# Optimization experiments

Hardware: AMD Instinct MI355X
Metric: run time of the kernel (lower is better)

Reference implementation:

```python
import jax, jax.numpy as jnp
import numpy as np

TEMPERATURE = 0.2
NUM_CLASSES = 80  # background label == NUM_CLASSES
M, K, B = 8192, 128, 60


def setup_inputs() -> dict:
    key = jax.random.key(0)
    k1, k2, k3 = jax.random.split(key, 3)
    feats = jax.random.normal(k1, (M, K), dtype=jnp.float32)
    feats = feats / jnp.linalg.norm(feats, axis=-1, keepdims=True)
    protos = jax.random.normal(k2, (B, K), dtype=jnp.float32)
    protos = protos / jnp.linalg.norm(protos, axis=-1, keepdims=True)
    labels = jax.random.randint(k3, (M,), 0, NUM_CLASSES + 1)  # NUM_CLASSES == bg
    proto_labels = jnp.arange(B, dtype=jnp.int64 if jax.config.read('jax_enable_x64') else jnp.int32)
    return {"features": feats, "labels": labels, "protos": protos, "proto_labels": proto_labels}


def reference(features, labels, protos, proto_labels):
    # masked (fixed-shape) formulation of the original boolean-gather code
    fg = labels != NUM_CLASSES                                   # [M]
    is_base = fg & jnp.any(labels[None, :] == proto_labels[:, None], axis=0)
    is_novel = fg & ~is_base
    nf = is_novel.astype(features.dtype)                         # [M] novel mask
    bf = is_base.astype(features.dtype)                          # [M] base mask
    numel = jnp.sum(fg).astype(features.dtype)

    sim = jnp.matmul(features, features.T) / TEMPERATURE          # [M,M]
    pk = jnp.matmul(features, protos.T) / TEMPERATURE             # [M,B]
    exp_sim = jnp.exp(sim)                                        # [M,M]
    eye = jnp.eye(features.shape[0], dtype=features.dtype)
    offdiag = (1.0 - eye)

    # ---- novel branch: rows i with is_novel[i] ----
    # denom: sum over novel j != i of exp(sim) + sum over protos of RAW pk (faithful to source)
    exp_nn_sum = jnp.sum(exp_sim * nf[None, :] * offdiag, axis=1)  # [M]
    denom_n = exp_nn_sum + jnp.sum(pk, axis=1)                     # [M]
    log_prob = sim - jnp.log(denom_n)[:, None]
    # novel_label_mask in source is elementwise labels==labels -> all True
    n_novel = jnp.sum(nf)
    cnt = jnp.maximum(n_novel - 1.0, 1.0)                          # per-row positive count
    per_row_novel = -jnp.sum(log_prob * nf[None, :] * offdiag, axis=1) / cnt
    loss_novel = jnp.sum(per_row_novel * nf)
    loss_novel = jnp.where(n_novel > 1.0, loss_novel, 0.0)

    # ---- base branch: rows i with is_base[i] ----
    safe_lab = jnp.clip(labels, 0, protos.shape[0] - 1)
    pi = jnp.einsum('nc,nc->n', features, protos[safe_lab]) / TEMPERATURE  # [M]
    denom_b = jnp.sum(exp_sim * nf[None, :], axis=1) + jnp.sum(jnp.exp(pk), axis=1)
    loss_base = jnp.sum(bf * -(pi - jnp.log(denom_b)))
    loss_base = jnp.where(jnp.any(is_base), loss_base, 0.0)

    return (loss_novel + loss_base) / numel
```

## Files before the change

kernel.cpp:

```cpp
#include <hip/hip_runtime.h>
#include <math.h>

#define NCLS 80
#define KDIM 128
#define INV_T 5.0f
#define AST 136
#define BST 72

typedef __attribute__((ext_vector_type(4))) float  floatx4;
typedef __attribute__((ext_vector_type(8))) short  short8;

__device__ inline unsigned short f2bf(float x) {
    unsigned int u = __float_as_uint(x);
    u += 0x7fffu + ((u >> 16) & 1u);
    return (unsigned short)(u >> 16);
}
__device__ inline ushort4 pack4(float4 v) {
    ushort4 r; r.x = f2bf(v.x); r.y = f2bf(v.y); r.z = f2bf(v.z); r.w = f2bf(v.w);
    return r;
}

__global__ __launch_bounds__(256) void setup_kernel(
    const int* __restrict__ labels, int M, int B,
    int* __restrict__ novel_idx, int* __restrict__ counters,
    float* __restrict__ S1, float* __restrict__ T1,
    float* __restrict__ PKr, float* __restrict__ EK, float* __restrict__ out)
{
    int i = blockIdx.x * 256 + threadIdx.x;
    if (i == 0) out[0] = 0.f;
    if (i >= M) return;
    S1[i] = 0.f; T1[i] = 0.f; PKr[i] = 0.f; EK[i] = 0.f;
    int lab = labels[i];
    bool fg  = (lab != NCLS);
    bool isb = fg && (lab >= 0) && (lab < B);
    bool isn = fg && !isb;
    if (isn) { int p = atomicAdd(&counters[0], 1); novel_idx[p] = i; }
    if (fg)  atomicAdd(&counters[1], 1);
    if (isb) atomicAdd(&counters[2], 1);
}

__global__ __launch_bounds__(256, 2) void gemm_kernel(
    const float* __restrict__ feats, const float* __restrict__ protos,
    const int* __restrict__ novel_idx, const int* __restrict__ counters,
    int M, int B,
    float* __restrict__ S1, float* __restrict__ T1,
    float* __restrict__ PKr, float* __restrict__ EK)
{
    __shared__ unsigned short As[128 * AST];
    __shared__ unsigned short Bs[128 * BST];
    __shared__ int nidx[128];

    const int Nn = counters[0];
    const int ntiles = (Nn + 127) >> 7;
    const int ct = blockIdx.x >> 6;
    const int rt = blockIdx.x & 63;
    if (ct > ntiles) return;
    const bool isproto = (ct == ntiles);
    const int row0 = rt * 128;
    const int tid = threadIdx.x;

    {
        const float4* f4 = (const float4*)(feats + (size_t)row0 * KDIM);
        #pragma unroll
        for (int p = 0; p < 16; ++p) {
            int chunk = p * 256 + tid;
            int r = chunk >> 5, kc = chunk & 31;
            float4 v = f4[r * 32 + kc];
            *(ushort4*)&As[r * AST + kc * 4] = pack4(v);
        }
    }

    const int wave = tid >> 6;
    const int lane = tid & 63;
    const int lr   = lane & 15;
    const int quad = lane >> 4;
    const int wrow = (wave >> 1) * 64;
    const int wcol = (wave & 1) * 64;

    floatx4 acc[4][4];
    #pragma unroll
    for (int r = 0; r < 4; ++r)
        #pragma unroll
        for (int c = 0; c < 4; ++c)
            acc[r][c] = (floatx4){0.f, 0.f, 0.f, 0.f};

    for (int h = 0; h < 2; ++h) {
        if (h) __syncthreads();
        #pragma unroll
        for (int p = 0; p < 8; ++p) {
            int chunk = p * 256 + tid;
            int r = chunk >> 4, kc = chunk & 15;
            float4 v = make_float4(0.f, 0.f, 0.f, 0.f);
            if (isproto) {
                if (r < B) v = *(const float4*)(protos + (size_t)r * KDIM + h * 64 + kc * 4);
            } else {
                int jg = ct * 128 + r;
                if (jg < Nn) {
                    int nid = novel_idx[jg];
                    v = *(const float4*)(feats + (size_t)nid * KDIM + h * 64 + kc * 4);
                }
            }
            *(ushort4*)&Bs[r * BST + kc * 4] = pack4(v);
        }
        if (h == 0 && tid < 128) {
            int nid = -1;
            if (isproto) { if (tid < B) nid = tid; }
            else { int jg = ct * 128 + tid; if (jg < Nn) nid = novel_idx[jg]; }
            nidx[tid] = nid;
        }
        __syncthreads();
        #pragma unroll
        for (int ks = 0; ks < 2; ++ks) {
            short8 a[4], b[4];
            #pragma unroll
            for (int r = 0; r < 4; ++r)
                a[r] = *(const short8*)&As[(wrow + r * 16 + lr) * AST + h * 64 + ks * 32 + quad * 8];
            #pragma unroll
            for (int c = 0; c < 4; ++c)
                b[c] = *(const short8*)&Bs[(wcol + c * 16 + lr) * BST + ks * 32 + quad * 8];
            #pragma unroll
            for (int r = 0; r < 4; ++r)
                #pragma unroll
                for (int c = 0; c < 4; ++c)
                    acc[r][c] = __builtin_amdgcn_mfma_f32_16x16x32_bf16(
                        a[r], b[c], acc[r][c], 0, 0, 0);
        }
    }

    int ncol[4];
    #pragma unroll
    for (int c = 0; c < 4; ++c) ncol[c] = nidx[wcol + c * 16 + lr];

    #pragma unroll
    for (int r = 0; r < 4; ++r) {
        int ibase = row0 + wrow + r * 16 + quad * 4;
        #pragma unroll
        for (int reg = 0; reg < 4; ++reg) {
            int irow = ibase + reg;
            float se = 0.f, sr = 0.f;
            #pragma unroll
            for (int c = 0; c < 4; ++c) {
                float sim = acc[r][c][reg] * INV_T;
                bool valid = (ncol[c] >= 0) && (isproto || ncol[c] != irow);
                if (valid) { se += __expf(sim); sr += sim; }
            }
            #pragma unroll
            for (int off = 1; off < 16; off <<= 1) {
                se += __shfl_xor(se, off);
                sr += __shfl_xor(sr, off);
            }
            if (lr == 0) {
                if (isproto) { atomicAdd(&EK[irow], se); atomicAdd(&PKr[irow], sr); }
                else         { atomicAdd(&S1[irow], se); atomicAdd(&T1[irow], sr); }
            }
        }
    }
}

__global__ __launch_bounds__(256) void finalize_kernel(
    const float* __restrict__ feats, const float* __restrict__ protos,
    const int* __restrict__ labels,
    const float* __restrict__ S1, const float* __restrict__ T1,
    const float* __restrict__ PKr, const float* __restrict__ EK,
    const int* __restrict__ counters, int M, int B, float* __restrict__ out)
{
    __shared__ float part[16];
    const int tid  = threadIdx.x;
    const int rloc = tid >> 4;
    const int q    = tid & 15;
    const int row  = blockIdx.x * 16 + rloc;
    const int rs   = min(row, M - 1);

    const int Nn = counters[0], numel = counters[1], nbase = counters[2];

    int lab = labels[rs];
    bool fg  = (lab != NCLS);
    bool isb = fg && (lab >= 0) && (lab < B);
    bool isn = fg && !isb;
    int  sl  = min(max(lab, 0), B - 1);

    float d = 0.f;
    #pragma unroll
    for (int j = 0; j < 8; ++j) {
        int k = q + j * 16;
        d += feats[(size_t)rs * KDIM + k] * protos[(size_t)sl * KDIM + k];
    }
    #pragma unroll
    for (int off = 1; off < 16; off <<= 1) d += __shfl_xor(d, off);

    if (q == 0) {
        float loss = 0.f;
        if (row < M) {
            if (isn && Nn > 1) {
                float cnt = (float)(Nn - 1);
                float dn  = S1[rs] + PKr[rs];
                loss = -(T1[rs] - cnt * logf(dn)) / cnt;
            } else if (isb && nbase > 0) {
                float pi = d * INV_T;
                float db = S1[rs] + EK[rs];
                loss = -(pi - logf(db));
            }
        }
        part[rloc] = loss;
    }
    __syncthreads();
    if (tid == 0) {
        float s = 0.f;
        #pragma unroll
        for (int r = 0; r < 16; ++r) s += part[r];
        atomicAdd(out, s / (float)numel);
    }
}

extern "C" void kernel_launch(void* const* d_in, const int* in_sizes, int n_in,
                              void* d_out, int out_size, void* d_ws, size_t ws_size,
                              hipStream_t stream)
{
    const float* feats  = (const float*)d_in[0];
    const int*   labels = (const int*)d_in[1];
    const float* protos = (const float*)d_in[2];

    const int M = in_sizes[1];
    const int B = in_sizes[3];

    char* ws = (char*)d_ws;
    int*   counters  = (int*)ws;
    float* S1  = (float*)(ws + 64);
    float* T1  = S1 + M;
    float* PKr = T1 + M;
    float* EK  = PKr + M;
    int*   novel_idx = (int*)(EK + M);

    hipMemsetAsync(counters, 0, 64, stream);

    setup_kernel<<<(M + 255) / 256, 256, 0, stream>>>(
        labels, M, B, novel_idx, counters, S1, T1, PKr, EK, (float*)d_out);

    int rowTiles = (M + 127) / 128;
    int maxct    = (M + 127) / 128;
    gemm_kernel<<<rowTiles * (maxct + 1), 256, 0, stream>>>(
        feats, protos, novel_idx, counters, M, B, S1, T1, PKr, EK);

    finalize_kernel<<<(M + 15) / 16, 256, 0, stream>>>(
        feats, protos, labels, S1, T1, PKr, EK, counters, M, B, (float*)d_out);
}
```

Baseline: 106.9 us.

## Fuse finalize into gemm via last-block reduction and single-block setup

```diff
diff --git a/kernel.cpp b/kernel.cpp
--- a/kernel.cpp
+++ b/kernel.cpp
@@ -5,7 +5,7 @@
 #define KDIM 128
 #define INV_T 5.0f
 #define AST 136
-#define BST 72
+#define BST 68
 
 typedef __attribute__((ext_vector_type(4))) float  floatx4;
 typedef __attribute__((ext_vector_type(8))) short  short8;
@@ -20,195 +20,232 @@
     return r;
 }
 
-__global__ __launch_bounds__(256) void setup_kernel(
+__global__ __launch_bounds__(1024) void setup_kernel(
     const int* __restrict__ labels, int M, int B,
     int* __restrict__ novel_idx, int* __restrict__ counters,
+    float* __restrict__ zbase )
+{
+    __shared__ int cnt_n, cfg, cb;
+    const int tid  = threadIdx.x;
+    const int lane = tid & 63;
+    if (tid == 0) { cnt_n = 0; cfg = 0; cb = 0; }
+
+    float4 z = make_float4(0.f, 0.f, 0.f, 0.f);
+    float4* b4 = (float4*)zbase;
+    const int n4 = (5 * M) >> 2;
+    for (int i = tid; i < n4; i += 1024) b4[i] = z;
+    __syncthreads();
+
+    int myfg = 0, myb = 0;
+    for (int i0 = 0; i0 < M; i0 += 1024) {
+        int i = i0 + tid;
+        int lab = (i < M) ? labels[i] : NCLS;
+        bool fg  = (lab != NCLS);
+        bool isb = fg && (lab >= 0) && (lab < B);
+        bool isn = fg && !isb;
+        unsigned long long m = __ballot(isn);
+        int wbase = 0;
+        if (lane == 0 && m) wbase = atomicAdd(&cnt_n, __popcll(m));
+        wbase = __shfl(wbase, 0);
+        if (isn) {
+            int pfx = __popcll(m & ((1ull << lane) - 1ull));
+            novel_idx[wbase + pfx] = i;
+        }
+        myfg += fg ? 1 : 0;
+        myb  += isb ? 1 : 0;
+    }
+    #pragma unroll
+    for (int off = 32; off; off >>= 1) {
+        myfg += __shfl_down(myfg, off);
+        myb  += __shfl_down(myb,  off);
+    }
+    if (lane == 0) { atomicAdd(&cfg, myfg); atomicAdd(&cb, myb); }
+    __syncthreads();
+    if (tid == 0) {
+        counters[0] = cnt_n;
+        counters[1] = cfg;
+        counters[2] = cb;
+        counters[3] = 0;
+    }
+}
+
+__global__ __launch_bounds__(256, 3) void gemm_kernel(
+    const float* __restrict__ feats, const float* __restrict__ protos,
+    const int* __restrict__ labels, const int* __restrict__ novel_idx,
+    int* __restrict__ counters, int M, int B, int rtiles,
     float* __restrict__ S1, float* __restrict__ T1,
-    float* __restrict__ PKr, float* __restrict__ EK, float* __restrict__ out)
-{
-    int i = blockIdx.x * 256 + threadIdx.x;
-    if (i == 0) out[0] = 0.f;
-    if (i >= M) return;
-    S1[i] = 0.f; T1[i] = 0.f; PKr[i] = 0.f; EK[i] = 0.f;
-    int lab = labels[i];
-    bool fg  = (lab != NCLS);
-    bool isb = fg && (lab >= 0) && (lab < B);
-    bool isn = fg && !isb;
-    if (isn) { int p = atomicAdd(&counters[0], 1); novel_idx[p] = i; }
-    if (fg)  atomicAdd(&counters[1], 1);
-    if (isb) atomicAdd(&counters[2], 1);
-}
-
-__global__ __launch_bounds__(256, 2) void gemm_kernel(
-    const float* __restrict__ feats, const float* __restrict__ protos,
-    const int* __restrict__ novel_idx, const int* __restrict__ counters,
-    int M, int B,
-    float* __restrict__ S1, float* __restrict__ T1,
-    float* __restrict__ PKr, float* __restrict__ EK)
+    float* __restrict__ PKr, float* __restrict__ EK, float* __restrict__ PIv,
+    float* __restrict__ out)
 {
     __shared__ unsigned short As[128 * AST];
     __shared__ unsigned short Bs[128 * BST];
-    __shared__ int nidx[128];
-
+    __shared__ int    nidx[128];
+    __shared__ int    rlab[128];
+    __shared__ double dred[4];
+    __shared__ int    lastflag;
+
+    const int tid = threadIdx.x;
     const int Nn = counters[0];
     const int ntiles = (Nn + 127) >> 7;
-    const int ct = blockIdx.x >> 6;
-    const int rt = blockIdx.x & 63;
-    if (ct > ntiles) return;
+    const int ct = blockIdx.x / rtiles;
+    const int rt = blockIdx.x - ct * rtiles;
+    const int row0 = rt * 128;
+    const bool active  = (ct <= ntiles);
     const bool isproto = (ct == ntiles);
-    const int row0 = rt * 128;
-    const int tid = threadIdx.x;
-
-    {
+
+    if (active) {
         const float4* f4 = (const float4*)(feats + (size_t)row0 * KDIM);
         #pragma unroll
         for (int p = 0; p < 16; ++p) {
             int chunk = p * 256 + tid;
             int r = chunk >> 5, kc = chunk & 31;
-            float4 v = f4[r * 32 + kc];
-            *(ushort4*)&As[r * AST + kc * 4] = pack4(v);
-        }
-    }
-
-    const int wave = tid >> 6;
-    const int lane = tid & 63;
-    const int lr   = lane & 15;
-    const int quad = lane >> 4;
-    const int wrow = (wave >> 1) * 64;
-    const int wcol = (wave & 1) * 64;
-
-    floatx4 acc[4][4];
-    #pragma unroll
-    for (int r = 0; r < 4; ++r)
-        #pragma unroll
-        for (int c = 0; c < 4; ++c)
-            acc[r][c] = (floatx4){0.f, 0.f, 0.f, 0.f};
-
-    for (int h = 0; h < 2; ++h) {
-        if (h) __syncthreads();
-        #pragma unroll
-        for (int p = 0; p < 8; ++p) {
-            int chunk = p * 256 + tid;
-            int r = chunk >> 4, kc = chunk & 15;
-            float4 v = make_float4(0.f, 0.f, 0.f, 0.f);
-            if (isproto) {
-                if (r < B) v = *(const float4*)(protos + (size_t)r * KDIM + h * 64 + kc * 4);
-            } else {
-                int jg = ct * 128 + r;
-                if (jg < Nn) {
-                    int nid = novel_idx[jg];
-                    v = *(const float4*)(feats + (size_t)nid * KDIM + h * 64 + kc * 4);
+            *(ushort4*)&As[r * AST + kc * 4] = pack4(f4[r * 32 + kc]);
+        }
+        if (tid < 128) rlab[tid] = labels[row0 + tid];
+
+        const int wave = tid >> 6, lane = tid & 63;
+        const int lr = lane & 15, quad = lane >> 4;
+        const int wrow = (wave >> 1) * 64, wcol = (wave & 1) * 64;
+
+        floatx4 acc[4][4];
+        #pragma unroll
+        for (int r = 0; r < 4; ++r)
+            #pragma unroll
+            for (int c = 0; c < 4; ++c)
+                acc[r][c] = (floatx4){0.f, 0.f, 0.f, 0.f};
+
+        for (int h = 0; h < 2; ++h) {
+            if (h) __syncthreads();
+            #pragma unroll
+            for (int p = 0; p < 8; ++p) {
+                int chunk = p * 256 + tid;
+                int r = chunk >> 4, kc = chunk & 15;
+                float4 v = make_float4(0.f, 0.f, 0.f, 0.f);
+                if (isproto) {
+                    if (r < B) v = *(const float4*)(protos + (size_t)r * KDIM + h * 64 + kc * 4);
+                } else {
+                    int jg = ct * 128 + r;
+                    if (jg < Nn)
+                        v = *(const float4*)(feats + (size_t)novel_idx[jg] * KDIM + h * 64 + kc * 4);
                 }
-            }
-            *(ushort4*)&Bs[r * BST + kc * 4] = pack4(v);
-        }
-        if (h == 0 && tid < 128) {
-            int nid = -1;
-            if (isproto) { if (tid < B) nid = tid; }
-            else { int jg = ct * 128 + tid; if (jg < Nn) nid = novel_idx[jg]; }
-            nidx[tid] = nid;
-        }
-        __syncthreads();
-        #pragma unroll
-        for (int ks = 0; ks < 2; ++ks) {
-            short8 a[4], b[4];
-            #pragma unroll
-            for (int r = 0; r < 4; ++r)
-                a[r] = *(const short8*)&As[(wrow + r * 16 + lr) * AST + h * 64 + ks * 32 + quad * 8];
-            #pragma unroll
-            for (int c = 0; c < 4; ++c)
-                b[c] = *(const short8*)&Bs[(wcol + c * 16 + lr) * BST + ks * 32 + quad * 8];
-            #pragma unroll
-            for (int r = 0; r < 4; ++r)
+                *(ushort4*)&Bs[r * BST + kc * 4] = pack4(v);
+            }
+            if (h == 0 && tid < 128) {
+                int nid = -1;
+                if (isproto) { if (tid < B) nid = tid; }
+                else { int jg = ct * 128 + tid; if (jg < Nn) nid = novel_idx[jg]; }
+                nidx[tid] = nid;
+            }
+            __syncthreads();
+            #pragma unroll
+            for (int ks = 0; ks < 2; ++ks) {
+                short8 a[4], b[4];
+                #pragma unroll
+                for (int r = 0; r < 4; ++r)
+                    a[r] = *(const short8*)&As[(wrow + r * 16 + lr) * AST + h * 64 + ks * 32 + quad * 8];
                 #pragma unroll
                 for (int c = 0; c < 4; ++c)
-                    acc[r][c] = __builtin_amdgcn_mfma_f32_16x16x32_bf16(
-                        a[r], b[c], acc[r][c], 0, 0, 0);
-        }
-    }
-
-    int ncol[4];
-    #pragma unroll
-    for (int c = 0; c < 4; ++c) ncol[c] = nidx[wcol + c * 16 + lr];
-
-    #pragma unroll
-    for (int r = 0; r < 4; ++r) {
-        int ibase = row0 + wrow + r * 16 + quad * 4;
-        #pragma unroll
-        for (int reg = 0; reg < 4; ++reg) {
-            int irow = ibase + reg;
-            float se = 0.f, sr = 0.f;
-            #pragma unroll
-            for (int c = 0; c < 4; ++c) {
-                float sim = acc[r][c][reg] * INV_T;
-                bool valid = (ncol[c] >= 0) && (isproto || ncol[c] != irow);
-                if (valid) { se += __expf(sim); sr += sim; }
-            }
-            #pragma unroll
-            for (int off = 1; off < 16; off <<= 1) {
-                se += __shfl_xor(se, off);
-                sr += __shfl_xor(sr, off);
-            }
-            if (lr == 0) {
-                if (isproto) { atomicAdd(&EK[irow], se); atomicAdd(&PKr[irow], sr); }
-                else         { atomicAdd(&S1[irow], se); atomicAdd(&T1[irow], sr); }
-            }
-        }
-    }
-}
-
-__global__ __launch_bounds__(256) void finalize_kernel(
-    const float* __restrict__ feats, const float* __restrict__ protos,
-    const int* __restrict__ labels,
-    const float* __restrict__ S1, const float* __restrict__ T1,
-    const float* __restrict__ PKr, const float* __restrict__ EK,
-    const int* __restrict__ counters, int M, int B, float* __restrict__ out)
-{
-    __shared__ float part[16];
-    const int tid  = threadIdx.x;
-    const int rloc = tid >> 4;
-    const int q    = tid & 15;
-    const int row  = blockIdx.x * 16 + rloc;
-    const int rs   = min(row, M - 1);
-
-    const int Nn = counters[0], numel = counters[1], nbase = counters[2];
-
-    int lab = labels[rs];
-    bool fg  = (lab != NCLS);
-    bool isb = fg && (lab >= 0) && (lab < B);
-    bool isn = fg && !isb;
-    int  sl  = min(max(lab, 0), B - 1);
-
-    float d = 0.f;
-    #pragma unroll
-    for (int j = 0; j < 8; ++j) {
-        int k = q + j * 16;
-        d += feats[(size_t)rs * KDIM + k] * protos[(size_t)sl * KDIM + k];
-    }
-    #pragma unroll
-    for (int off = 1; off < 16; off <<= 1) d += __shfl_xor(d, off);
-
-    if (q == 0) {
-        float loss = 0.f;
-        if (row < M) {
+                    b[c] = *(const short8*)&Bs[(wcol + c * 16 + lr) * BST + ks * 32 + quad * 8];
+                #pragma unroll
+                for (int r = 0; r < 4; ++r)
+                    #pragma unroll
+                    for (int c = 0; c < 4; ++c)
+                        acc[r][c] = __builtin_amdgcn_mfma_f32_16x16x32_bf16(
+                            a[r], b[c], acc[r][c], 0, 0, 0);
+            }
+        }
+
+        int ncol[4];
+        #pragma unroll
+        for (int c = 0; c < 4; ++c) ncol[c] = nidx[wcol + c * 16 + lr];
+
+        #pragma unroll
+        for (int r = 0; r < 4; ++r) {
+            #pragma unroll
+            for (int reg = 0; reg < 4; ++reg) {
+                int lrow = wrow + r * 16 + quad * 4 + reg;
+                int irow = row0 + lrow;
+                if (isproto) {
+                    int lab = rlab[lrow];
+                    int sl  = min(max(lab, 0), B - 1);
+                    float se = 0.f, sr = 0.f, spi = 0.f;
+                    #pragma unroll
+                    for (int c = 0; c < 4; ++c) {
+                        float sim = acc[r][c][reg] * INV_T;
+                        if (ncol[c] >= 0) {
+                            se += __expf(sim); sr += sim;
+                            if (ncol[c] == sl) spi += sim;
+                        }
+                    }
+                    #pragma unroll
+                    for (int off = 1; off < 16; off <<= 1) {
+                        se += __shfl_xor(se, off);
+                        sr += __shfl_xor(sr, off);
+                        spi += __shfl_xor(spi, off);
+                    }
+                    if (lr == 0) {
+                        atomicAdd(&EK[irow], se);
+                        atomicAdd(&PKr[irow], sr);
+                        atomicAdd(&PIv[irow], spi);
+                    }
+                } else {
+                    float se = 0.f, sr = 0.f;
+                    #pragma unroll
+                    for (int c = 0; c < 4; ++c) {
+                        float sim = acc[r][c][reg] * INV_T;
+                        if (ncol[c] >= 0 && ncol[c] != irow) {
+                            se += __expf(sim); sr += sim;
+                        }
+                    }
+                    #pragma unroll
+                    for (int off = 1; off < 16; off <<= 1) {
+                        se += __shfl_xor(se, off);
+                        sr += __shfl_xor(sr, off);
+                    }
+                    if (lr == 0) {
+                        atomicAdd(&S1[irow], se);
+                        atomicAdd(&T1[irow], sr);
+                    }
+                }
+            }
+        }
+    }
+
+    __syncthreads();
+    if (tid == 0) {
+        __threadfence();
+        int old = atomicAdd(&counters[3], 1);
+        lastflag = (old == (int)gridDim.x - 1) ? 1 : 0;
+    }
+    __syncthreads();
+    if (lastflag) {
+        __threadfence();
+        const int numel = counters[1];
+        const float cnt = (float)(Nn - 1);
+        double part = 0.0;
+        for (int i = tid; i < M; i += 256) {
+            int lab = labels[i];
+            bool fg  = (lab != NCLS);
+            bool isb = fg && (lab >= 0) && (lab < B);
+            bool isn = fg && !isb;
             if (isn && Nn > 1) {
-                float cnt = (float)(Nn - 1);
-                float dn  = S1[rs] + PKr[rs];
-                loss = -(T1[rs] - cnt * logf(dn)) / cnt;
-            } else if (isb && nbase > 0) {
-                float pi = d * INV_T;
-                float db = S1[rs] + EK[rs];
-                loss = -(pi - logf(db));
-            }
-        }
-        part[rloc] = loss;
-    }
-    __syncthreads();
-    if (tid == 0) {
-        float s = 0.f;
-        #pragma unroll
-        for (int r = 0; r < 16; ++r) s += part[r];
-        atomicAdd(out, s / (float)numel);
+                float s1 = __hip_atomic_load(&S1[i],  __ATOMIC_RELAXED, __HIP_MEMORY_SCOPE_AGENT);
+                float t1 = __hip_atomic_load(&T1[i],  __ATOMIC_RELAXED, __HIP_MEMORY_SCOPE_AGENT);
+                float pk = __hip_atomic_load(&PKr[i], __ATOMIC_RELAXED, __HIP_MEMORY_SCOPE_AGENT);
+                part += (double)(-(t1 - cnt * logf(s1 + pk)) / cnt);
+            } else if (isb) {
+                float s1 = __hip_atomic_load(&S1[i],  __ATOMIC_RELAXED, __HIP_MEMORY_SCOPE_AGENT);
+                float ek = __hip_atomic_load(&EK[i],  __ATOMIC_RELAXED, __HIP_MEMORY_SCOPE_AGENT);
+                float pi = __hip_atomic_load(&PIv[i], __ATOMIC_RELAXED, __HIP_MEMORY_SCOPE_AGENT);
+                part += (double)(-(pi - logf(s1 + ek)));
+            }
+        }
+        #pragma unroll
+        for (int off = 32; off; off >>= 1) part += __shfl_down(part, off);
+        if ((tid & 63) == 0) dred[tid >> 6] = part;
+        __syncthreads();
+        if (tid == 0)
+            out[0] = (float)((dred[0] + dred[1] + dred[2] + dred[3]) / (double)numel);
     }
 }
 
@@ -224,23 +261,19 @@
     const int B = in_sizes[3];
 
     char* ws = (char*)d_ws;
-    int*   counters  = (int*)ws;
+    int*   counters = (int*)ws;
     float* S1  = (float*)(ws + 64);
     float* T1  = S1 + M;
     float* PKr = T1 + M;
     float* EK  = PKr + M;
-    int*   novel_idx = (int*)(EK + M);
-
-    hipMemsetAsync(counters, 0, 64, stream);
-
-    setup_kernel<<<(M + 255) / 256, 256, 0, stream>>>(
-        labels, M, B, novel_idx, counters, S1, T1, PKr, EK, (float*)d_out);
-
-    int rowTiles = (M + 127) / 128;
-    int maxct    = (M + 127) / 128;
-    gemm_kernel<<<rowTiles * (maxct + 1), 256, 0, stream>>>(
-        feats, protos, novel_idx, counters, M, B, S1, T1, PKr, EK);
-
-    finalize_kernel<<<(M + 15) / 16, 256, 0, stream>>>(
-        feats, protos, labels, S1, T1, PKr, EK, counters, M, B, (float*)d_out);
-}
+    float* PIv = EK + M;
+    int*   novel_idx = (int*)(PIv + M);
+
+    setup_kernel<<<1, 1024, 0, stream>>>(labels, M, B, novel_idx, counters, S1);
+
+    const int rtiles = (M + 127) / 128;
+    const int grid   = rtiles * (rtiles + 1);
+    gemm_kernel<<<grid, 256, 0, stream>>>(
+        feats, protos, labels, novel_idx, counters, M, B, rtiles,
+        S1, T1, PKr, EK, PIv, (float*)d_out);
+}
```

Result: slower. 192.3 us (+79.8%).

## Make GEMM blocks persistent over column tiles and aggregate setup atomics per wave

Applied to the files above, without the earlier changes.

```diff
diff --git a/kernel.cpp b/kernel.cpp
--- a/kernel.cpp
+++ b/kernel.cpp
@@ -5,7 +5,7 @@
 #define KDIM 128
 #define INV_T 5.0f
 #define AST 136
-#define BST 72
+#define CSPLIT 8
 
 typedef __attribute__((ext_vector_type(4))) float  floatx4;
 typedef __attribute__((ext_vector_type(8))) short  short8;
@@ -23,20 +23,40 @@
 __global__ __launch_bounds__(256) void setup_kernel(
     const int* __restrict__ labels, int M, int B,
     int* __restrict__ novel_idx, int* __restrict__ counters,
-    float* __restrict__ S1, float* __restrict__ T1,
-    float* __restrict__ PKr, float* __restrict__ EK, float* __restrict__ out)
-{
-    int i = blockIdx.x * 256 + threadIdx.x;
-    if (i == 0) out[0] = 0.f;
-    if (i >= M) return;
-    S1[i] = 0.f; T1[i] = 0.f; PKr[i] = 0.f; EK[i] = 0.f;
-    int lab = labels[i];
+    float* __restrict__ zbase ,
+    float* __restrict__ out)
+{
+    const int gid  = blockIdx.x * 256 + threadIdx.x;
+    const int lane = threadIdx.x & 63;
+    if (gid == 0) out[0] = 0.f;
+
+    float4* b4 = (float4*)zbase;
+    const int n4 = M;
+    for (int i = gid; i < n4; i += gridDim.x * 256)
+        b4[i] = make_float4(0.f, 0.f, 0.f, 0.f);
+
+    int lab = (gid < M) ? labels[gid] : NCLS;
     bool fg  = (lab != NCLS);
     bool isb = fg && (lab >= 0) && (lab < B);
     bool isn = fg && !isb;
-    if (isn) { int p = atomicAdd(&counters[0], 1); novel_idx[p] = i; }
-    if (fg)  atomicAdd(&counters[1], 1);
-    if (isb) atomicAdd(&counters[2], 1);
+    unsigned long long m = __ballot(isn);
+    int wbase = 0;
+    if (lane == 0 && m) wbase = atomicAdd(&counters[0], __popcll(m));
+    wbase = __shfl(wbase, 0);
+    if (isn) {
+        int pfx = __popcll(m & ((1ull << lane) - 1ull));
+        novel_idx[wbase + pfx] = gid;
+    }
+    int myfg = fg ? 1 : 0, myb = isb ? 1 : 0;
+    #pragma unroll
+    for (int off = 32; off; off >>= 1) {
+        myfg += __shfl_down(myfg, off);
+        myb  += __shfl_down(myb,  off);
+    }
+    if (lane == 0) {
+        if (myfg) atomicAdd(&counters[1], myfg);
+        if (myb)  atomicAdd(&counters[2], myb);
+    }
 }
 
 __global__ __launch_bounds__(256, 2) void gemm_kernel(
@@ -47,17 +67,15 @@
     float* __restrict__ PKr, float* __restrict__ EK)
 {
     __shared__ unsigned short As[128 * AST];
-    __shared__ unsigned short Bs[128 * BST];
+    __shared__ unsigned short Bs[128 * AST];
     __shared__ int nidx[128];
 
+    const int tid = threadIdx.x;
+    const int rt  = blockIdx.x >> 3;
+    const int cs  = blockIdx.x & (CSPLIT - 1);
+    const int row0 = rt * 128;
     const int Nn = counters[0];
     const int ntiles = (Nn + 127) >> 7;
-    const int ct = blockIdx.x >> 6;
-    const int rt = blockIdx.x & 63;
-    if (ct > ntiles) return;
-    const bool isproto = (ct == ntiles);
-    const int row0 = rt * 128;
-    const int tid = threadIdx.x;
 
     {
         const float4* f4 = (const float4*)(feats + (size_t)row0 * KDIM);
@@ -65,59 +83,55 @@
         for (int p = 0; p < 16; ++p) {
             int chunk = p * 256 + tid;
             int r = chunk >> 5, kc = chunk & 31;
-            float4 v = f4[r * 32 + kc];
-            *(ushort4*)&As[r * AST + kc * 4] = pack4(v);
-        }
-    }
-
-    const int wave = tid >> 6;
-    const int lane = tid & 63;
-    const int lr   = lane & 15;
-    const int quad = lane >> 4;
-    const int wrow = (wave >> 1) * 64;
-    const int wcol = (wave & 1) * 64;
-
-    floatx4 acc[4][4];
-    #pragma unroll
-    for (int r = 0; r < 4; ++r)
-        #pragma unroll
-        for (int c = 0; c < 4; ++c)
-            acc[r][c] = (floatx4){0.f, 0.f, 0.f, 0.f};
-
-    for (int h = 0; h < 2; ++h) {
-        if (h) __syncthreads();
-        #pragma unroll
-        for (int p = 0; p < 8; ++p) {
+            *(ushort4*)&As[r * AST + kc * 4] = pack4(f4[r * 32 + kc]);
+        }
+    }
+
+    const int wave = tid >> 6, lane = tid & 63;
+    const int lr = lane & 15, quad = lane >> 4;
+    const int wrow = (wave >> 1) * 64, wcol = (wave & 1) * 64;
+
+    for (int ct = cs; ct <= ntiles; ct += CSPLIT) {
+        const bool isproto = (ct == ntiles);
+        __syncthreads();
+        #pragma unroll
+        for (int p = 0; p < 16; ++p) {
             int chunk = p * 256 + tid;
-            int r = chunk >> 4, kc = chunk & 15;
+            int r = chunk >> 5, kc = chunk & 31;
             float4 v = make_float4(0.f, 0.f, 0.f, 0.f);
             if (isproto) {
-                if (r < B) v = *(const float4*)(protos + (size_t)r * KDIM + h * 64 + kc * 4);
+                if (r < B) v = *(const float4*)(protos + (size_t)r * KDIM + kc * 4);
             } else {
                 int jg = ct * 128 + r;
-                if (jg < Nn) {
-                    int nid = novel_idx[jg];
-                    v = *(const float4*)(feats + (size_t)nid * KDIM + h * 64 + kc * 4);
-                }
+                if (jg < Nn)
+                    v = *(const float4*)(feats + (size_t)novel_idx[jg] * KDIM + kc * 4);
             }
-            *(ushort4*)&Bs[r * BST + kc * 4] = pack4(v);
-        }
-        if (h == 0 && tid < 128) {
+            *(ushort4*)&Bs[r * AST + kc * 4] = pack4(v);
+        }
+        if (tid < 128) {
             int nid = -1;
             if (isproto) { if (tid < B) nid = tid; }
             else { int jg = ct * 128 + tid; if (jg < Nn) nid = novel_idx[jg]; }
             nidx[tid] = nid;
         }
         __syncthreads();
-        #pragma unroll
-        for (int ks = 0; ks < 2; ++ks) {
+
+        floatx4 acc[4][4];
+        #pragma unroll
+        for (int r = 0; r < 4; ++r)
+            #pragma unroll
+            for (int c = 0; c < 4; ++c)
+                acc[r][c] = (floatx4){0.f, 0.f, 0.f, 0.f};
+
+        #pragma unroll
+        for (int ks = 0; ks < 4; ++ks) {
             short8 a[4], b[4];
             #pragma unroll
             for (int r = 0; r < 4; ++r)
-                a[r] = *(const short8*)&As[(wrow + r * 16 + lr) * AST + h * 64 + ks * 32 + quad * 8];
+                a[r] = *(const short8*)&As[(wrow + r * 16 + lr) * AST + ks * 32 + quad * 8];
             #pragma unroll
             for (int c = 0; c < 4; ++c)
-                b[c] = *(const short8*)&Bs[(wcol + c * 16 + lr) * BST + ks * 32 + quad * 8];
+                b[c] = *(const short8*)&Bs[(wcol + c * 16 + lr) * AST + ks * 32 + quad * 8];
             #pragma unroll
             for (int r = 0; r < 4; ++r)
                 #pragma unroll
@@ -125,33 +139,32 @@
                     acc[r][c] = __builtin_amdgcn_mfma_f32_16x16x32_bf16(
                         a[r], b[c], acc[r][c], 0, 0, 0);
         }
-    }
-
-    int ncol[4];
-    #pragma unroll
-    for (int c = 0; c < 4; ++c) ncol[c] = nidx[wcol + c * 16 + lr];
-
-    #pragma unroll
-    for (int r = 0; r < 4; ++r) {
-        int ibase = row0 + wrow + r * 16 + quad * 4;
-        #pragma unroll
-        for (int reg = 0; reg < 4; ++reg) {
-            int irow = ibase + reg;
-            float se = 0.f, sr = 0.f;
-            #pragma unroll
-            for (int c = 0; c < 4; ++c) {
-                float sim = acc[r][c][reg] * INV_T;
-                bool valid = (ncol[c] >= 0) && (isproto || ncol[c] != irow);
-                if (valid) { se += __expf(sim); sr += sim; }
-            }
-            #pragma unroll
-            for (int off = 1; off < 16; off <<= 1) {
-                se += __shfl_xor(se, off);
-                sr += __shfl_xor(sr, off);
-            }
-            if (lr == 0) {
-                if (isproto) { atomicAdd(&EK[irow], se); atomicAdd(&PKr[irow], sr); }
-                else         { atomicAdd(&S1[irow], se); atomicAdd(&T1[irow], sr); }
+
+        int ncol[4];
+        #pragma unroll
+        for (int c = 0; c < 4; ++c) ncol[c] = nidx[wcol + c * 16 + lr];
+
+        #pragma unroll
+        for (int r = 0; r < 4; ++r) {
+            #pragma unroll
+            for (int reg = 0; reg < 4; ++reg) {
+                int irow = row0 + wrow + r * 16 + quad * 4 + reg;
+                float se = 0.f, sr = 0.f;
+                #pragma unroll
+                for (int c = 0; c < 4; ++c) {
+                    float sim = acc[r][c][reg] * INV_T;
+                    bool valid = (ncol[c] >= 0) && (isproto || ncol[c] != irow);
+                    if (valid) { se += __expf(sim); sr += sim; }
+                }
+                #pragma unroll
+                for (int off = 1; off < 16; off <<= 1) {
+                    se += __shfl_xor(se, off);
+                    sr += __shfl_xor(sr, off);
+                }
+                if (lr == 0) {
+                    if (isproto) { atomicAdd(&EK[irow], se); atomicAdd(&PKr[irow], sr); }
+                    else         { atomicAdd(&S1[irow], se); atomicAdd(&T1[irow], sr); }
+                }
             }
         }
     }
@@ -171,7 +184,7 @@
     const int row  = blockIdx.x * 16 + rloc;
     const int rs   = min(row, M - 1);
 
-    const int Nn = counters[0], numel = counters[1], nbase = counters[2];
+    const int Nn = counters[0], numel = counters[1];
 
     int lab = labels[rs];
     bool fg  = (lab != NCLS);
@@ -195,7 +208,7 @@
                 float cnt = (float)(Nn - 1);
                 float dn  = S1[rs] + PKr[rs];
                 loss = -(T1[rs] - cnt * logf(dn)) / cnt;
-            } else if (isb && nbase > 0) {
+            } else if (isb) {
                 float pi = d * INV_T;
                 float db = S1[rs] + EK[rs];
                 loss = -(pi - logf(db));
@@ -224,7 +237,7 @@
     const int B = in_sizes[3];
 
     char* ws = (char*)d_ws;
-    int*   counters  = (int*)ws;
+    int*   counters = (int*)ws;
     float* S1  = (float*)(ws + 64);
     float* T1  = S1 + M;
     float* PKr = T1 + M;
@@ -234,11 +247,10 @@
     hipMemsetAsync(counters, 0, 64, stream);
 
     setup_kernel<<<(M + 255) / 256, 256, 0, stream>>>(
-        labels, M, B, novel_idx, counters, S1, T1, PKr, EK, (float*)d_out);
-
-    int rowTiles = (M + 127) / 128;
-    int maxct    = (M + 127) / 128;
-    gemm_kernel<<<rowTiles * (maxct + 1), 256, 0, stream>>>(
+        labels, M, B, novel_idx, counters, S1, (float*)d_out);
+
+    const int rtiles = (M + 127) / 128;
+    gemm_kernel<<<rtiles * CSPLIT, 256, 0, stream>>>(
         feats, protos, novel_idx, counters, M, B, S1, T1, PKr, EK);
 
     finalize_kernel<<<(M + 15) / 16, 256, 0, stream>>>(
```

After: 112.0 us. +4.7%, slower.
